# Kernel optimization log

Hardware: AMD Instinct MI355X
Metric: run time of the kernel (lower is better)

Reference implementation:

```python
import jax, jax.numpy as jnp
import numpy as np

B, N, ENC = 64, 49, 2048
DEC, ATT, EMB, V, TP1 = 512, 512, 300, 10000, 31


def setup_inputs() -> dict:
    key = jax.random.key(0)
    ks = jax.random.split(key, 20)
    s = 0.02
    inp = {
        "features": jax.random.normal(ks[0], (B, N, ENC), jnp.float32),
        "captions": jax.random.randint(ks[1], (B, TP1), 0, V, jnp.int64),
        "emb": jax.random.normal(ks[2], (V, EMB), jnp.float32) * s,
        "U_w": jax.random.normal(ks[3], (ATT, ENC), jnp.float32) * s,
        "U_b": jnp.zeros((ATT,), jnp.float32),
        "W_w": jax.random.normal(ks[4], (ATT, DEC), jnp.float32) * s,
        "W_b": jnp.zeros((ATT,), jnp.float32),
        "A_w": jax.random.normal(ks[5], (1, ATT), jnp.float32) * s,
        "A_b": jnp.zeros((1,), jnp.float32),
        "initH_w": jax.random.normal(ks[6], (DEC, ENC), jnp.float32) * s,
        "initH_b": jnp.zeros((DEC,), jnp.float32),
        "initC_w": jax.random.normal(ks[7], (DEC, ENC), jnp.float32) * s,
        "initC_b": jnp.zeros((DEC,), jnp.float32),
        "ih_w": jax.random.normal(ks[8], (4 * DEC, EMB + ENC), jnp.float32) * s,
        "ih_b": jnp.zeros((4 * DEC,), jnp.float32),
        "hh_w": jax.random.normal(ks[9], (4 * DEC, DEC), jnp.float32) * s,
        "hh_b": jnp.zeros((4 * DEC,), jnp.float32),
        "fcn_w": jax.random.normal(ks[10], (V, DEC), jnp.float32) * s,
        "fcn_b": jnp.zeros((V,), jnp.float32),
    }
    return inp


def reference(features, captions, emb, U_w, U_b, W_w, W_b, A_w, A_b,
              initH_w, initH_b, initC_w, initC_b,
              ih_w, ih_b, hh_w, hh_b, fcn_w, fcn_b):
    # embeds: [B, T+1, EMB]  (prembed lookup, frozen table)
    embeds = emb[captions]
    T = captions.shape[1] - 1  # static

    # init_hidden_state
    mean_f = features.mean(axis=1)                  # [B, ENC]
    h0 = mean_f @ initH_w.T + initH_b               # [B, DEC]
    c0 = mean_f @ initC_w.T + initC_b

    # U(features) is step-invariant: hoist out of the loop (same math)
    u_hs = jnp.einsum('bne,ae->bna', features, U_w) + U_b  # [B, N, ATT]

    xs = jnp.swapaxes(embeds[:, :T], 0, 1)          # [T, B, EMB]

    def step(carry, x):
        h, c = carry
        # additive attention
        w_ah = h @ W_w.T + W_b                       # [B, ATT]
        comb = jnp.tanh(u_hs + w_ah[:, None, :])     # [B, N, ATT]
        scores = jnp.einsum('bna,a->bn', comb, A_w[0]) + A_b[0]
        alpha = jax.nn.softmax(scores, axis=1)       # [B, N]
        context = jnp.einsum('bn,bne->be', alpha, features)  # [B, ENC]
        # LSTMCell
        lstm_in = jnp.concatenate([x, context], axis=1)
        gates = lstm_in @ ih_w.T + ih_b + h @ hh_w.T + hh_b
        i, f, g, o = jnp.split(gates, 4, axis=1)
        i, f, o = jax.nn.sigmoid(i), jax.nn.sigmoid(f), jax.nn.sigmoid(o)
        g = jnp.tanh(g)
        c = f * c + i * g
        h = o * jnp.tanh(c)
        # dropout in eval mode = identity
        out = h @ fcn_w.T + fcn_b                    # [B, V]
        return (h, c), (out, alpha)

    _, (preds, alphas) = jax.lax.scan(step, (h0, c0), xs)
    preds = jnp.swapaxes(preds, 0, 1)                # [B, T, V]
    alphas = jnp.swapaxes(alphas, 0, 1)              # [B, T, N]
    return preds, alphas
```

## Files before the change

### kernel.cpp

```cpp
#include <hip/hip_runtime.h>
#include <math.h>

#define B 64
#define NN 49
#define ENC 2048
#define DEC 512
#define ATT 512
#define EMB 300
#define VOC 10000
#define TT 30

typedef __attribute__((ext_vector_type(4))) float f32x4;
typedef __attribute__((ext_vector_type(4))) short s16x4;
typedef __attribute__((ext_vector_type(8))) short s16x8;
typedef unsigned short u16;

__device__ __forceinline__ float fast_tanh(float x) {
    float e = __expf(2.f * x);
    return 1.f - 2.f / (e + 1.f);
}
__device__ __forceinline__ float sigmoidf(float x) {
    return 1.f / (1.f + __expf(-x));
}
__device__ __forceinline__ u16 f2bf(float x) {
    unsigned u = __float_as_uint(x);
    unsigned r = u + 0x7FFFu + ((u >> 16) & 1u);
    return (u16)(r >> 16);
}
__device__ __forceinline__ float bf2f(u16 u) {
    return __uint_as_float((unsigned)u << 16);
}
__device__ __forceinline__ void split_bf16(float x, short& hi, short& lo) {
    u16 h = f2bf(x);
    float hf = __uint_as_float((unsigned)h << 16);
    hi = (short)h;
    lo = (short)f2bf(x - hf);
}
__device__ __forceinline__ s16x8 ld8(const short* p) {
    s16x4 a = *(const s16x4*)p;
    s16x4 b = *(const s16x4*)(p + 4);
    return __builtin_shufflevector(a, b, 0, 1, 2, 3, 4, 5, 6, 7);
}

__global__ __launch_bounds__(512) void mfma_nt(
    const float* __restrict__ A, int lda,
    const float* __restrict__ Bm, int ldb,
    const float* __restrict__ bias,
    float* __restrict__ C, int ldc,
    int M, int N, int K, int mode)
{
    __shared__ short Ah[128][40];
    __shared__ short Al[128][40];
    __shared__ short Bh[128][40];
    __shared__ short Bl[128][40];

    const int tid = threadIdx.x;
    const int m0 = blockIdx.y * 128, n0 = blockIdx.x * 128;
    const int wid = tid >> 6, lane = tid & 63;
    const int wm = wid >> 2, wn = wid & 3;
    const int lrow = lane & 15;
    const int lko = (lane >> 4) * 8;
    const int srow = tid >> 2;
    const int sk = (tid & 3) * 8;

    f32x4 acc[4][2];
    #pragma unroll
    for (int i = 0; i < 4; ++i)
        #pragma unroll
        for (int j = 0; j < 2; ++j)
            acc[i][j] = (f32x4){0.f, 0.f, 0.f, 0.f};

    const int nkt = (K + 31) >> 5;
    for (int kt = 0; kt < nkt; ++kt) {
        const int kb0 = kt * 32 + sk;
        {
            const int gr = m0 + srow;
            float v[8];
            if (gr < M && kb0 + 7 < K) {
                const float* p = A + (size_t)gr * lda + kb0;
                float4 x0 = *(const float4*)p;
                float4 x1 = *(const float4*)(p + 4);
                v[0] = x0.x; v[1] = x0.y; v[2] = x0.z; v[3] = x0.w;
                v[4] = x1.x; v[5] = x1.y; v[6] = x1.z; v[7] = x1.w;
            } else {
                #pragma unroll
                for (int j = 0; j < 8; ++j)
                    v[j] = (gr < M && kb0 + j < K) ? A[(size_t)gr * lda + kb0 + j] : 0.f;
            }
            s16x4 h0, h1, l0, l1;
            #pragma unroll
            for (int j = 0; j < 4; ++j) { short h, l; split_bf16(v[j], h, l); h0[j] = h; l0[j] = l; }
            #pragma unroll
            for (int j = 0; j < 4; ++j) { short h, l; split_bf16(v[4 + j], h, l); h1[j] = h; l1[j] = l; }
            *(s16x4*)&Ah[srow][sk] = h0; *(s16x4*)&Ah[srow][sk + 4] = h1;
            *(s16x4*)&Al[srow][sk] = l0; *(s16x4*)&Al[srow][sk + 4] = l1;
        }
        {
            const int gc = n0 + srow;
            float v[8];
            if (gc < N && kb0 + 7 < K) {
                const float* p = Bm + (size_t)gc * ldb + kb0;
                float4 x0 = *(const float4*)p;
                float4 x1 = *(const float4*)(p + 4);
                v[0] = x0.x; v[1] = x0.y; v[2] = x0.z; v[3] = x0.w;
                v[4] = x1.x; v[5] = x1.y; v[6] = x1.z; v[7] = x1.w;
            } else {
                #pragma unroll
                for (int j = 0; j < 8; ++j)
                    v[j] = (gc < N && kb0 + j < K) ? Bm[(size_t)gc * ldb + kb0 + j] : 0.f;
            }
            s16x4 h0, h1, l0, l1;
            #pragma unroll
            for (int j = 0; j < 4; ++j) { short h, l; split_bf16(v[j], h, l); h0[j] = h; l0[j] = l; }
            #pragma unroll
            for (int j = 0; j < 4; ++j) { short h, l; split_bf16(v[4 + j], h, l); h1[j] = h; l1[j] = l; }
            *(s16x4*)&Bh[srow][sk] = h0; *(s16x4*)&Bh[srow][sk + 4] = h1;
            *(s16x4*)&Bl[srow][sk] = l0; *(s16x4*)&Bl[srow][sk + 4] = l1;
        }
        __syncthreads();

        s16x8 bh[2], bl[2];
        #pragma unroll
        for (int nr = 0; nr < 2; ++nr) {
            const int col = wn * 32 + nr * 16 + lrow;
            bh[nr] = ld8(&Bh[col][lko]);
            bl[nr] = ld8(&Bl[col][lko]);
        }
        #pragma unroll
        for (int mr = 0; mr < 4; ++mr) {
            const int row = wm * 64 + mr * 16 + lrow;
            s16x8 ah = ld8(&Ah[row][lko]);
            s16x8 al = ld8(&Al[row][lko]);
            #pragma unroll
            for (int nr = 0; nr < 2; ++nr) {
                acc[mr][nr] = __builtin_amdgcn_mfma_f32_16x16x32_bf16(ah, bh[nr], acc[mr][nr], 0, 0, 0);
                acc[mr][nr] = __builtin_amdgcn_mfma_f32_16x16x32_bf16(ah, bl[nr], acc[mr][nr], 0, 0, 0);
                acc[mr][nr] = __builtin_amdgcn_mfma_f32_16x16x32_bf16(al, bh[nr], acc[mr][nr], 0, 0, 0);
            }
        }
        __syncthreads();
    }

    #pragma unroll
    for (int mr = 0; mr < 4; ++mr) {
        #pragma unroll
        for (int nr = 0; nr < 2; ++nr) {
            #pragma unroll
            for (int r = 0; r < 4; ++r) {
                const int row = m0 + wm * 64 + mr * 16 + (lane >> 4) * 4 + r;
                const int col = n0 + wn * 32 + nr * 16 + (lane & 15);
                if (row < M && col < N) {
                    float val = acc[mr][nr][r] + (bias ? bias[col] : 0.f);
                    if (mode == 0) C[(size_t)row * ldc + col] = val;
                    else if (mode == 1) {
                        const int t = row >> 6, bb = row & 63;
                        C[(size_t)bb * (TT * VOC) + (size_t)t * VOC + col] = val;
                    } else {
                        ((u16*)C)[(size_t)row * ldc + col] = f2bf(val);
                    }
                }
            }
        }
    }
}

__global__ __launch_bounds__(512) void mfma_pre(
    const u16* __restrict__ Ahg, const u16* __restrict__ Alg,
    const u16* __restrict__ Bhg, const u16* __restrict__ Blg,
    const float* __restrict__ bias,
    float* __restrict__ C, int M, int N)
{
    __shared__ short Ah[128][40];
    __shared__ short Al[128][40];
    __shared__ short Bh[128][40];
    __shared__ short Bl[128][40];

    const int tid = threadIdx.x;
    const int m0 = blockIdx.y * 128, n0 = blockIdx.x * 128;
    const int wid = tid >> 6, lane = tid & 63;
    const int wm = wid >> 2, wn = wid & 3;
    const int lrow = lane & 15;
    const int lko = (lane >> 4) * 8;
    const int srow = tid >> 2;
    const int sk = (tid & 3) * 8;

    f32x4 acc[4][2];
    #pragma unroll
    for (int i = 0; i < 4; ++i)
        #pragma unroll
        for (int j = 0; j < 2; ++j)
            acc[i][j] = (f32x4){0.f, 0.f, 0.f, 0.f};

    for (int kt = 0; kt < 16; ++kt) {
        const int kb0 = kt * 32 + sk;
        {
            const int gr = m0 + srow;
            s16x8 vh = {0,0,0,0,0,0,0,0}, vl = {0,0,0,0,0,0,0,0};
            if (gr < M) {
                vh = *(const s16x8*)(Ahg + (size_t)gr * 512 + kb0);
                vl = *(const s16x8*)(Alg + (size_t)gr * 512 + kb0);
            }
            *(s16x8*)&Ah[srow][sk] = vh;
            *(s16x8*)&Al[srow][sk] = vl;
        }
        {
            const int gc = n0 + srow;
            s16x8 vh = {0,0,0,0,0,0,0,0}, vl = {0,0,0,0,0,0,0,0};
            if (gc < N) {
                vh = *(const s16x8*)(Bhg + (size_t)gc * 512 + kb0);
                vl = *(const s16x8*)(Blg + (size_t)gc * 512 + kb0);
            }
            *(s16x8*)&Bh[srow][sk] = vh;
            *(s16x8*)&Bl[srow][sk] = vl;
        }
        __syncthreads();

        s16x8 bh[2], bl[2];
        #pragma unroll
        for (int nr = 0; nr < 2; ++nr) {
            const int col = wn * 32 + nr * 16 + lrow;
            bh[nr] = ld8(&Bh[col][lko]);
            bl[nr] = ld8(&Bl[col][lko]);
        }
        #pragma unroll
        for (int mr = 0; mr < 4; ++mr) {
            const int row = wm * 64 + mr * 16 + lrow;
            s16x8 ah = ld8(&Ah[row][lko]);
            s16x8 al = ld8(&Al[row][lko]);
            #pragma unroll
            for (int nr = 0; nr < 2; ++nr) {
                acc[mr][nr] = __builtin_amdgcn_mfma_f32_16x16x32_bf16(ah, bh[nr], acc[mr][nr], 0, 0, 0);
                acc[mr][nr] = __builtin_amdgcn_mfma_f32_16x16x32_bf16(ah, bl[nr], acc[mr][nr], 0, 0, 0);
                acc[mr][nr] = __builtin_amdgcn_mfma_f32_16x16x32_bf16(al, bh[nr], acc[mr][nr], 0, 0, 0);
            }
        }
        __syncthreads();
    }

    #pragma unroll
    for (int mr = 0; mr < 4; ++mr) {
        #pragma unroll
        for (int nr = 0; nr < 2; ++nr) {
            #pragma unroll
            for (int r = 0; r < 4; ++r) {
                const int row = m0 + wm * 64 + mr * 16 + (lane >> 4) * 4 + r;
                const int col = n0 + wn * 32 + nr * 16 + (lane & 15);
                if (row < M && col < N) {
                    const float val = acc[mr][nr][r] + bias[col];
                    const int t = row >> 6, bb = row & 63;
                    C[(size_t)bb * (TT * VOC) + (size_t)t * VOC + col] = val;
                }
            }
        }
    }
}

__global__ __launch_bounds__(256) void k_mean(const float* __restrict__ f,
                                              float* __restrict__ mean_f)
{
    const int b = blockIdx.x;
    for (int e = threadIdx.x; e < ENC; e += 256) {
        float s = 0.f;
        for (int n = 0; n < NN; ++n) s += f[(size_t)(b * NN + n) * ENC + e];
        mean_f[(size_t)b * ENC + e] = s * (1.f / 49.f);
    }
}

__global__ __launch_bounds__(256) void k_init_partial(
    const float* __restrict__ mean_f,
    const float* __restrict__ iH_w, const float* __restrict__ iC_w,
    float* __restrict__ pbuf)
{
    const int tid = threadIdx.x;
    const int tx = tid & 15, ty = tid >> 4;
    const int n0 = blockIdx.x * 64;
    const int ks = blockIdx.y;
    __shared__ float As[16][64];
    __shared__ float Bs[16][64];
    float acc[4][4] = {};
    const int lrow = tid >> 2;
    const int lk = (tid & 3) * 4;
    for (int c = 0; c < 8; ++c) {
        const int kk = ks * 128 + c * 16 + lk;
        float4 av = *(const float4*)(mean_f + (size_t)lrow * 2048 + kk);
        const int col = n0 + lrow;
        const float* wp = (col < 512) ? (iH_w + (size_t)col * 2048)
                                      : (iC_w + (size_t)(col - 512) * 2048);
        float4 bv = *(const float4*)(wp + kk);
        As[lk + 0][lrow] = av.x; As[lk + 1][lrow] = av.y;
        As[lk + 2][lrow] = av.z; As[lk + 3][lrow] = av.w;
        Bs[lk + 0][lrow] = bv.x; Bs[lk + 1][lrow] = bv.y;
        Bs[lk + 2][lrow] = bv.z; Bs[lk + 3][lrow] = bv.w;
        __syncthreads();
        #pragma unroll
        for (int k = 0; k < 16; ++k) {
            float4 a = *(const float4*)&As[k][ty * 4];
            float4 b = *(const float4*)&Bs[k][tx * 4];
            acc[0][0] += a.x * b.x; acc[0][1] += a.x * b.y; acc[0][2] += a.x * b.z; acc[0][3] += a.x * b.w;
            acc[1][0] += a.y * b.x; acc[1][1] += a.y * b.y; acc[1][2] += a.y * b.z; acc[1][3] += a.y * b.w;
            acc[2][0] += a.z * b.x; acc[2][1] += a.z * b.y; acc[2][2] += a.z * b.z; acc[2][3] += a.z * b.w;
            acc[3][0] += a.w * b.x; acc[3][1] += a.w * b.y; acc[3][2] += a.w * b.z; acc[3][3] += a.w * b.w;
        }
        __syncthreads();
    }
    #pragma unroll
    for (int i = 0; i < 4; ++i) {
        const int r = ty * 4 + i;
        #pragma unroll
        for (int j = 0; j < 4; ++j)
            pbuf[(size_t)(ks * 64 + r) * 1024 + n0 + tx * 4 + j] = acc[i][j];
    }
}

__global__ __launch_bounds__(256) void k_init_reduce(
    const float* __restrict__ pbuf,
    const float* __restrict__ iH_b, const float* __restrict__ iC_b,
    float* __restrict__ h_cur, float* __restrict__ c_cur)
{
    const int idx = blockIdx.x * 256 + threadIdx.x;
    const int r = idx >> 10, c = idx & 1023;
    float s = 0.f;
    #pragma unroll
    for (int ks = 0; ks < 16; ++ks) s += pbuf[(size_t)(ks * 64 + r) * 1024 + c];
    if (c < 512) h_cur[r * 512 + c] = s + iH_b[c];
    else         c_cur[r * 512 + (c - 512)] = s + iC_b[c - 512];
}

__global__ __launch_bounds__(256) void k_embed(const int* __restrict__ cap,
                                               const float* __restrict__ emb,
                                               float* __restrict__ embeds)
{
    const int r = blockIdx.x;
    const int t = r >> 6, b = r & 63;
    const int c = cap[b * 31 + t];
    for (int j = threadIdx.x; j < EMB; j += 256)
        embeds[(size_t)r * EMB + j] = emb[(size_t)c * EMB + j];
}

__global__ void k_bias2(const float* __restrict__ a, const float* __restrict__ b,
                        float* __restrict__ o)
{
    const int j = blockIdx.x * 256 + threadIdx.x;
    if (j < 2048) o[j] = a[j] + b[j];
}

__global__ __launch_bounds__(256) void k_split(const float* __restrict__ src,
                                               u16* __restrict__ hi, u16* __restrict__ lo,
                                               int n)
{
    const int i = (blockIdx.x * 256 + threadIdx.x) * 4;
    if (i >= n) return;
    f32x4 v = *(const f32x4*)(src + i);
    s16x4 h4, l4;
    #pragma unroll
    for (int j = 0; j < 4; ++j) { short h, l; split_bf16(v[j], h, l); h4[j] = h; l4[j] = l; }
    *(s16x4*)(hi + i) = h4;
    *(s16x4*)(lo + i) = l4;
}

__global__ __launch_bounds__(256) void k_hw4(
    const float* __restrict__ h,
    const float* __restrict__ W_w, const float* __restrict__ W_b,
    const float* __restrict__ hh_w,
    float* __restrict__ wahp, float* __restrict__ ghhp)
{
    const int tid = threadIdx.x;
    const int tx = tid & 15, ty = tid >> 4;
    const int n0 = blockIdx.x * 64;
    const int ks = blockIdx.y;
    const float* Bp; const float* biasp; float* Cp; int c0, ldc;
    if (n0 < 512) { Bp = W_w + (size_t)n0 * 512; biasp = (ks == 0) ? W_b : nullptr; Cp = wahp + (size_t)ks * 32768; c0 = n0; ldc = 512; }
    else { Bp = hh_w + (size_t)(n0 - 512) * 512; biasp = nullptr; Cp = ghhp + (size_t)ks * 131072; c0 = n0 - 512; ldc = 2048; }

    __shared__ float As[64][68];
    __shared__ float Bs[64][68];
    float acc[4][4] = {};
    const int rt = tid >> 2;
    const int cs = (tid & 3) * 16;

    for (int kh = 0; kh < 2; ++kh) {
        const int kbase = ks * 128 + kh * 64;
        #pragma unroll
        for (int i = 0; i < 4; ++i) {
            const int c = cs + i * 4;
            *(f32x4*)&As[rt][c] = *(const f32x4*)(h + (size_t)rt * 512 + kbase + c);
            *(f32x4*)&Bs[rt][c] = *(const f32x4*)(Bp + (size_t)rt * 512 + kbase + c);
        }
        __syncthreads();
        #pragma unroll
        for (int k4 = 0; k4 < 16; ++k4) {
            f32x4 a0 = *(const f32x4*)&As[ty * 4 + 0][k4 * 4];
            f32x4 a1 = *(const f32x4*)&As[ty * 4 + 1][k4 * 4];
            f32x4 a2 = *(const f32x4*)&As[ty * 4 + 2][k4 * 4];
            f32x4 a3 = *(const f32x4*)&As[ty * 4 + 3][k4 * 4];
            f32x4 b0 = *(const f32x4*)&Bs[tx * 4 + 0][k4 * 4];
            f32x4 b1 = *(const f32x4*)&Bs[tx * 4 + 1][k4 * 4];
            f32x4 b2 = *(const f32x4*)&Bs[tx * 4 + 2][k4 * 4];
            f32x4 b3 = *(const f32x4*)&Bs[tx * 4 + 3][k4 * 4];
            #pragma unroll
            for (int e = 0; e < 4; ++e) {
                acc[0][0] += a0[e] * b0[e]; acc[0][1] += a0[e] * b1[e];
                acc[0][2] += a0[e] * b2[e]; acc[0][3] += a0[e] * b3[e];
                acc[1][0] += a1[e] * b0[e]; acc[1][1] += a1[e] * b1[e];
                acc[1][2] += a1[e] * b2[e]; acc[1][3] += a1[e] * b3[e];
                acc[2][0] += a2[e] * b0[e]; acc[2][1] += a2[e] * b1[e];
                acc[2][2] += a2[e] * b2[e]; acc[2][3] += a2[e] * b3[e];
                acc[3][0] += a3[e] * b0[e]; acc[3][1] += a3[e] * b1[e];
                acc[3][2] += a3[e] * b2[e]; acc[3][3] += a3[e] * b3[e];
            }
        }
        __syncthreads();
    }
    #pragma unroll
    for (int i = 0; i < 4; ++i) {
        const int r = ty * 4 + i;
        #pragma unroll
        for (int j = 0; j < 4; ++j) {
            const int cc = c0 + tx * 4 + j;
            Cp[(size_t)r * ldc + cc] = acc[i][j] + (biasp ? biasp[cc] : 0.f);
        }
    }
}

__global__ __launch_bounds__(512) void k_fused3(
    const u16* __restrict__ uhs16,
    const float* __restrict__ A_w, const float* __restrict__ A_b,
    const float* __restrict__ wahp,
    const float* __restrict__ ghhp,
    const float* __restrict__ pre_x,
    const u16* __restrict__ fW16,
    float* __restrict__ h_cur, float* __restrict__ c_cur,
    u16* __restrict__ Hall_h, u16* __restrict__ Hall_l,
    float* __restrict__ alphas, int s)
{
    const int bb = blockIdx.x;
    const int qq = blockIdx.y;
    const int tid = threadIdx.x;
    const int lane = tid & 63, w = tid >> 6;
    __shared__ float wah_l[512];
    __shared__ float awl[512];
    __shared__ float red[64];
    __shared__ float al[64];
    __shared__ float ghl[512];
    __shared__ float gl[512];

    const int gate = tid >> 7, dloc = tid & 127;
    const int jcol = gate * 512 + qq * 128 + dloc;
    float ghv = pre_x[(size_t)(s * 64 + bb) * 2048 + jcol]
              + ghhp[(size_t)bb * 2048 + jcol]
              + ghhp[131072 + (size_t)bb * 2048 + jcol]
              + ghhp[262144 + (size_t)bb * 2048 + jcol]
              + ghhp[393216 + (size_t)bb * 2048 + jcol];
    float wv = wahp[bb * 512 + tid] + wahp[32768 + bb * 512 + tid]
             + wahp[65536 + bb * 512 + tid] + wahp[98304 + bb * 512 + tid];
    const float cload = c_cur[bb * 512 + qq * 128 + (tid & 127)];

    const int ngf = tid & 7, r = tid >> 3;
    const int gf = r >> 4, oc = r & 15;
    const int jb = gf * 512 + qq * 128 + oc * 8;
    const u16* fb = fW16 + (size_t)bb * NN * 2048 + jb;
    s16x8 pf[7];
    #pragma unroll
    for (int i = 0; i < 7; ++i) {
        const int n = ngf + 8 * i;
        if (n < NN) pf[i] = *(const s16x8*)(fb + (size_t)n * 2048);
        else        pf[i] = (s16x8){0, 0, 0, 0, 0, 0, 0, 0};
    }

    ghl[tid] = ghv;
    wah_l[tid] = wv;
    awl[tid] = A_w[tid];
    __syncthreads();

    for (int n = w; n < NN; n += 8) {
        const u16* up = uhs16 + (size_t)(bb * NN + n) * 512;
        float acc = 0.f;
        #pragma unroll
        for (int i = 0; i < 8; ++i) {
            const int a = lane + i * 64;
            acc += awl[a] * fast_tanh(bf2f(up[a]) + wah_l[a]);
        }
        #pragma unroll
        for (int m = 32; m; m >>= 1) acc += __shfl_xor(acc, m, 64);
        if (lane == 0) red[n] = acc + A_b[0];
    }
    __syncthreads();

    if (tid < 64) {
        const float sc = (tid < NN) ? red[tid] : -1e30f;
        float mx = sc;
        #pragma unroll
        for (int m = 32; m; m >>= 1) mx = fmaxf(mx, __shfl_xor(mx, m, 64));
        float e = (tid < NN) ? __expf(sc - mx) : 0.f;
        float sum = e;
        #pragma unroll
        for (int m = 32; m; m >>= 1) sum += __shfl_xor(sum, m, 64);
        const float av = e / sum;
        al[tid] = av;
        if (qq == 0 && tid < NN)
            alphas[(size_t)bb * (TT * NN) + (size_t)s * NN + tid] = av;
    }
    __syncthreads();

    float a8[8] = {0.f, 0.f, 0.f, 0.f, 0.f, 0.f, 0.f, 0.f};
    #pragma unroll
    for (int i = 0; i < 7; ++i) {
        const int n = ngf + 8 * i;
        const float av = al[n];
        #pragma unroll
        for (int k = 0; k < 8; ++k)
            a8[k] += av * bf2f((u16)pf[i][k]);
    }
    #pragma unroll
    for (int m = 1; m < 8; m <<= 1)
        #pragma unroll
        for (int k = 0; k < 8; ++k)
            a8[k] += __shfl_xor(a8[k], m, 64);
    if (ngf == 0) {
        const int base = gf * 128 + oc * 8;
        #pragma unroll
        for (int k = 0; k < 8; ++k)
            gl[base + k] = a8[k] + ghl[base + k];
    }
    __syncthreads();

    if (tid < 128) {
        const int dd = qq * 128 + tid;
        const float ig = sigmoidf(gl[tid]);
        const float fg = sigmoidf(gl[128 + tid]);
        const float gg = fast_tanh(gl[256 + tid]);
        const float og = sigmoidf(gl[384 + tid]);
        const float cv = fg * cload + ig * gg;
        const float hv = og * fast_tanh(cv);
        c_cur[bb * 512 + dd] = cv;
        h_cur[bb * 512 + dd] = hv;
        short hh, hl;
        split_bf16(hv, hh, hl);
        Hall_h[(size_t)(s * 64 + bb) * 512 + dd] = (u16)hh;
        Hall_l[(size_t)(s * 64 + bb) * 512 + dd] = (u16)hl;
    }
}

extern "C" void kernel_launch(void* const* d_in, const int* in_sizes, int n_in,
                              void* d_out, int out_size, void* d_ws, size_t ws_size,
                              hipStream_t stream)
{
    const float* features = (const float*)d_in[0];
    const int*   captions = (const int*)d_in[1];
    const float* emb      = (const float*)d_in[2];
    const float* U_w      = (const float*)d_in[3];
    const float* U_b      = (const float*)d_in[4];
    const float* W_w      = (const float*)d_in[5];
    const float* W_b      = (const float*)d_in[6];
    const float* A_w      = (const float*)d_in[7];
    const float* A_b      = (const float*)d_in[8];
    const float* iH_w     = (const float*)d_in[9];
    const float* iH_b     = (const float*)d_in[10];
    const float* iC_w     = (const float*)d_in[11];
    const float* iC_b     = (const float*)d_in[12];
    const float* ih_w     = (const float*)d_in[13];
    const float* ih_b     = (const float*)d_in[14];
    const float* hh_w     = (const float*)d_in[15];
    const float* hh_b     = (const float*)d_in[16];
    const float* fcn_w    = (const float*)d_in[17];
    const float* fcn_b    = (const float*)d_in[18];

    float* out    = (float*)d_out;
    float* alphas = out + (size_t)B * TT * VOC;

    float* ws     = (float*)d_ws;
    u16*  fW16    = (u16*)ws;
    u16*  uhs16   = (u16*)(ws + 3211264);
    float* pre_x  = ws + 4014080;
    u16*  Hall_h  = (u16*)(ws + 7946240);
    u16*  Hall_l  = (u16*)(ws + 8437760);
    float* mean_f = ws + 8929280;
    float* h_cur  = ws + 9060352;
    float* c_cur  = ws + 9093120;
    float* wahp   = ws + 9125888;
    float* ghhp   = ws + 9256960;
    float* embeds = ws + 9781248;
    float* bias2  = ws + 10357248;
    float* pbuf   = ws;
    u16*  fcnw_h  = (u16*)pre_x;
    u16*  fcnw_l  = (u16*)ws;

    k_mean<<<64, 256, 0, stream>>>(features, mean_f);
    k_init_partial<<<dim3(16, 16), 256, 0, stream>>>(mean_f, iH_w, iC_w, pbuf);
    k_init_reduce<<<256, 256, 0, stream>>>(pbuf, iH_b, iC_b, h_cur, c_cur);

    k_embed<<<1920, 256, 0, stream>>>(captions, emb, embeds);
    k_bias2<<<8, 256, 0, stream>>>(ih_b, hh_b, bias2);
    mfma_nt<<<dim3(4, 25), 512, 0, stream>>>(features, ENC, U_w, ENC, U_b, (float*)uhs16, ATT, B * NN, ATT, ENC, 2);
    mfma_nt<<<dim3(16, 15), 512, 0, stream>>>(embeds, EMB, ih_w, 2348, bias2, pre_x, 2048, TT * B, 2048, EMB, 0);
    mfma_nt<<<dim3(16, 25), 512, 0, stream>>>(features, ENC, ih_w + 300, 2348, nullptr, (float*)fW16, 2048, B * NN, 2048, ENC, 2);

    k_hw4<<<dim3(40, 4), 256, 0, stream>>>(h_cur, W_w, W_b, hh_w, wahp, ghhp);
    for (int s = 0; s < TT; ++s) {
        k_fused3<<<dim3(64, 4), 512, 0, stream>>>(uhs16, A_w, A_b, wahp, ghhp, pre_x, fW16,
                                                  h_cur, c_cur, Hall_h, Hall_l, alphas, s);
        if (s < TT - 1)
            k_hw4<<<dim3(40, 4), 256, 0, stream>>>(h_cur, W_w, W_b, hh_w, wahp, ghhp);
    }

    k_split<<<5000, 256, 0, stream>>>(fcn_w, fcnw_h, fcnw_l, VOC * DEC);
    mfma_pre<<<dim3(79, 15), 512, 0, stream>>>(Hall_h, Hall_l, fcnw_h, fcnw_l, fcn_b,
                                               out, TT * B, VOC);
}
```

Baseline: 1.050 ms.

## Fuse U and ih feature projections into one GEMM with pre-split features

Result: faster. 925.1 us (-11.9%).

```diff
diff --git a/kernel.cpp b/kernel.cpp
--- a/kernel.cpp
+++ b/kernel.cpp
@@ -149,15 +149,107 @@
             for (int r = 0; r < 4; ++r) {
                 const int row = m0 + wm * 64 + mr * 16 + (lane >> 4) * 4 + r;
                 const int col = n0 + wn * 32 + nr * 16 + (lane & 15);
-                if (row < M && col < N) {
-                    float val = acc[mr][nr][r] + (bias ? bias[col] : 0.f);
-                    if (mode == 0) C[(size_t)row * ldc + col] = val;
-                    else if (mode == 1) {
-                        const int t = row >> 6, bb = row & 63;
-                        C[(size_t)bb * (TT * VOC) + (size_t)t * VOC + col] = val;
-                    } else {
-                        ((u16*)C)[(size_t)row * ldc + col] = f2bf(val);
-                    }
+                if (row < M && col < N)
+                    C[(size_t)row * ldc + col] = acc[mr][nr][r] + (bias ? bias[col] : 0.f);
+            }
+        }
+    }
+}
+
+__global__ __launch_bounds__(512) void mfma_cat(
+    const u16* __restrict__ fhi, const u16* __restrict__ flo,
+    const float* __restrict__ U_w, const float* __restrict__ U_b,
+    const float* __restrict__ ih_w,
+    u16* __restrict__ uhs16, u16* __restrict__ fW16, int M)
+{
+    __shared__ short Ah[128][40];
+    __shared__ short Al[128][40];
+    __shared__ short Bh[128][40];
+    __shared__ short Bl[128][40];
+
+    const int tid = threadIdx.x;
+    const int m0 = blockIdx.y * 128, n0 = blockIdx.x * 128;
+    const int wid = tid >> 6, lane = tid & 63;
+    const int wm = wid >> 2, wn = wid & 3;
+    const int lrow = lane & 15;
+    const int lko = (lane >> 4) * 8;
+    const int srow = tid >> 2;
+    const int sk = (tid & 3) * 8;
+
+    const int gc = n0 + srow;
+    const float* bp = (gc < 512) ? (U_w + (size_t)gc * 2048)
+                                 : (ih_w + (size_t)(gc - 512) * 2348 + 300);
+    const int gr = m0 + srow;
+    const u16* ahp = fhi + (size_t)gr * 2048;
+    const u16* alp = flo + (size_t)gr * 2048;
+
+    f32x4 acc[4][2];
+    #pragma unroll
+    for (int i = 0; i < 4; ++i)
+        #pragma unroll
+        for (int j = 0; j < 2; ++j)
+            acc[i][j] = (f32x4){0.f, 0.f, 0.f, 0.f};
+
+    for (int kt = 0; kt < 64; ++kt) {
+        const int kb0 = kt * 32 + sk;
+        {
+            s16x8 vh = {0,0,0,0,0,0,0,0}, vl = {0,0,0,0,0,0,0,0};
+            if (gr < M) {
+                vh = *(const s16x8*)(ahp + kb0);
+                vl = *(const s16x8*)(alp + kb0);
+            }
+            *(s16x8*)&Ah[srow][sk] = vh;
+            *(s16x8*)&Al[srow][sk] = vl;
+        }
+        {
+            float4 x0 = *(const float4*)(bp + kb0);
+            float4 x1 = *(const float4*)(bp + kb0 + 4);
+            float v[8] = {x0.x, x0.y, x0.z, x0.w, x1.x, x1.y, x1.z, x1.w};
+            s16x4 h0, h1, l0, l1;
+            #pragma unroll
+            for (int j = 0; j < 4; ++j) { short h, l; split_bf16(v[j], h, l); h0[j] = h; l0[j] = l; }
+            #pragma unroll
+            for (int j = 0; j < 4; ++j) { short h, l; split_bf16(v[4 + j], h, l); h1[j] = h; l1[j] = l; }
+            *(s16x4*)&Bh[srow][sk] = h0; *(s16x4*)&Bh[srow][sk + 4] = h1;
+            *(s16x4*)&Bl[srow][sk] = l0; *(s16x4*)&Bl[srow][sk + 4] = l1;
+        }
+        __syncthreads();
+
+        s16x8 bh[2], bl[2];
+        #pragma unroll
+        for (int nr = 0; nr < 2; ++nr) {
+            const int col = wn * 32 + nr * 16 + lrow;
+            bh[nr] = ld8(&Bh[col][lko]);
+            bl[nr] = ld8(&Bl[col][lko]);
+        }
+        #pragma unroll
+        for (int mr = 0; mr < 4; ++mr) {
+            const int row = wm * 64 + mr * 16 + lrow;
+            s16x8 ah = ld8(&Ah[row][lko]);
+            s16x8 al = ld8(&Al[row][lko]);
+            #pragma unroll
+            for (int nr = 0; nr < 2; ++nr) {
+                acc[mr][nr] = __builtin_amdgcn_mfma_f32_16x16x32_bf16(ah, bh[nr], acc[mr][nr], 0, 0, 0);
+                acc[mr][nr] = __builtin_amdgcn_mfma_f32_16x16x32_bf16(ah, bl[nr], acc[mr][nr], 0, 0, 0);
+                acc[mr][nr] = __builtin_amdgcn_mfma_f32_16x16x32_bf16(al, bh[nr], acc[mr][nr], 0, 0, 0);
+            }
+        }
+        __syncthreads();
+    }
+
+    #pragma unroll
+    for (int mr = 0; mr < 4; ++mr) {
+        #pragma unroll
+        for (int nr = 0; nr < 2; ++nr) {
+            #pragma unroll
+            for (int r = 0; r < 4; ++r) {
+                const int row = m0 + wm * 64 + mr * 16 + (lane >> 4) * 4 + r;
+                const int col = n0 + wn * 32 + nr * 16 + (lane & 15);
+                if (row < M) {
+                    if (col < 512)
+                        uhs16[(size_t)row * 512 + col] = f2bf(acc[mr][nr][r] + U_b[col]);
+                    else
+                        fW16[(size_t)row * 2048 + (col - 512)] = f2bf(acc[mr][nr][r]);
                 }
             }
         }
@@ -422,7 +514,7 @@
     }
 }
 
-__global__ __launch_bounds__(512) void k_fused3(
+__global__ __launch_bounds__(512) void k_fused4(
     const u16* __restrict__ uhs16,
     const float* __restrict__ A_w, const float* __restrict__ A_b,
     const float* __restrict__ wahp,
@@ -438,7 +530,6 @@
     const int tid = threadIdx.x;
     const int lane = tid & 63, w = tid >> 6;
     __shared__ float wah_l[512];
-    __shared__ float awl[512];
     __shared__ float red[64];
     __shared__ float al[64];
     __shared__ float ghl[512];
@@ -455,6 +546,11 @@
              + wahp[65536 + bb * 512 + tid] + wahp[98304 + bb * 512 + tid];
     const float cload = c_cur[bb * 512 + qq * 128 + (tid & 127)];
 
+    const int a0 = lane * 8;
+    float aw8[8];
+    #pragma unroll
+    for (int k = 0; k < 8; ++k) aw8[k] = A_w[a0 + k];
+
     const int ngf = tid & 7, r = tid >> 3;
     const int gf = r >> 4, oc = r & 15;
     const int jb = gf * 512 + qq * 128 + oc * 8;
@@ -469,20 +565,25 @@
 
     ghl[tid] = ghv;
     wah_l[tid] = wv;
-    awl[tid] = A_w[tid];
     __syncthreads();
 
-    for (int n = w; n < NN; n += 8) {
-        const u16* up = uhs16 + (size_t)(bb * NN + n) * 512;
+    float wh8[8];
+    #pragma unroll
+    for (int k = 0; k < 8; ++k) wh8[k] = wah_l[a0 + k];
+
+    const u16* ub = uhs16 + (size_t)(bb * NN) * 512 + a0;
+    #pragma unroll
+    for (int i = 0; i < 7; ++i) {
+        const int n = w + 8 * i;
+        const int nc = (n < NN) ? n : 0;
+        const s16x8 uv = *(const s16x8*)(ub + (size_t)nc * 512);
         float acc = 0.f;
         #pragma unroll
-        for (int i = 0; i < 8; ++i) {
-            const int a = lane + i * 64;
-            acc += awl[a] * fast_tanh(bf2f(up[a]) + wah_l[a]);
-        }
+        for (int k = 0; k < 8; ++k)
+            acc += aw8[k] * fast_tanh(bf2f((u16)uv[k]) + wh8[k]);
         #pragma unroll
         for (int m = 32; m; m >>= 1) acc += __shfl_xor(acc, m, 64);
-        if (lane == 0) red[n] = acc + A_b[0];
+        if (lane == 0 && n < NN) red[n] = acc + A_b[0];
     }
     __syncthreads();
 
@@ -581,9 +682,11 @@
     float* ghhp   = ws + 9256960;
     float* embeds = ws + 9781248;
     float* bias2  = ws + 10357248;
+    u16*  fhi     = (u16*)(ws + 10359296);
+    u16*  flo     = (u16*)(ws + 13570560);
     float* pbuf   = ws;
-    u16*  fcnw_h  = (u16*)pre_x;
-    u16*  fcnw_l  = (u16*)ws;
+    u16*  fcnw_h  = fhi;
+    u16*  fcnw_l  = flo;
 
     k_mean<<<64, 256, 0, stream>>>(features, mean_f);
     k_init_partial<<<dim3(16, 16), 256, 0, stream>>>(mean_f, iH_w, iC_w, pbuf);
@@ -591,13 +694,13 @@
 
     k_embed<<<1920, 256, 0, stream>>>(captions, emb, embeds);
     k_bias2<<<8, 256, 0, stream>>>(ih_b, hh_b, bias2);
-    mfma_nt<<<dim3(4, 25), 512, 0, stream>>>(features, ENC, U_w, ENC, U_b, (float*)uhs16, ATT, B * NN, ATT, ENC, 2);
+    k_split<<<6272, 256, 0, stream>>>(features, fhi, flo, B * NN * ENC);
+    mfma_cat<<<dim3(20, 25), 512, 0, stream>>>(fhi, flo, U_w, U_b, ih_w, uhs16, fW16, B * NN);
     mfma_nt<<<dim3(16, 15), 512, 0, stream>>>(embeds, EMB, ih_w, 2348, bias2, pre_x, 2048, TT * B, 2048, EMB, 0);
-    mfma_nt<<<dim3(16, 25), 512, 0, stream>>>(features, ENC, ih_w + 300, 2348, nullptr, (float*)fW16, 2048, B * NN, 2048, ENC, 2);
 
     k_hw4<<<dim3(40, 4), 256, 0, stream>>>(h_cur, W_w, W_b, hh_w, wahp, ghhp);
     for (int s = 0; s < TT; ++s) {
-        k_fused3<<<dim3(64, 4), 512, 0, stream>>>(uhs16, A_w, A_b, wahp, ghhp, pre_x, fW16,
+        k_fused4<<<dim3(64, 4), 512, 0, stream>>>(uhs16, A_w, A_b, wahp, ghhp, pre_x, fW16,
                                                   h_cur, c_cur, Hall_h, Hall_l, alphas, s);
         if (s < TT - 1)
             k_hw4<<<dim3(40, 4), 256, 0, stream>>>(h_cur, W_w, W_b, hh_w, wahp, ghhp);
```
